# Kernel optimization log

Hardware: AMD Instinct MI355X
Metric: run time of the kernel (lower is better)

## Reference

```python
import jax, jax.numpy as jnp
import numpy as np

B, LT, D, H, DI = 8, 128, 512, 8, 2048
NMEM, LMEM = 1024, 64
DH = D // H
EPS = 1e-5
NEG = -1e9

def _ln(x, g, b):
    mu = x.mean(-1, keepdims=True)
    var = ((x - mu) ** 2).mean(-1, keepdims=True)
    return (x - mu) * jax.lax.rsqrt(var + EPS) * g + b

def _ffn(x, W1, b1, W2, b2):
    # PositionwiseFF with residual=True (dropout=0 / eval)
    return x + jax.nn.relu(x @ W1 + b1) @ W2 + b2

def setup_inputs():
    key = jax.random.key(0)
    ks = jax.random.split(key, 16)
    w = lambda i, shape: jax.random.normal(ks[i], shape, jnp.float32) * 0.02
    return {
        "dec_output": jax.random.normal(ks[0], (B, LT, D), jnp.float32),
        "mem_attn_out": jax.random.normal(ks[1], (B, LT, NMEM + 1), jnp.float32),
        "enc_out_mem": jax.random.normal(ks[2], (NMEM, LMEM, D), jnp.float32),
        "tgt_emb_mem": jax.random.normal(ks[3], (NMEM, LMEM, D), jnp.float32),
        "tgt_mask_mem": jax.random.randint(ks[4], (NMEM, LMEM), 0, 2, jnp.int32),
        "tgt_mask": jax.random.randint(ks[5], (B, LT), 0, 2, jnp.int32),
        "g0": jnp.ones((D,), jnp.float32), "be0": jnp.zeros((D,), jnp.float32),
        "g1": jnp.ones((D,), jnp.float32), "be1": jnp.zeros((D,), jnp.float32),
        "Wq": w(6, (D, D)), "bq": jnp.zeros((D,), jnp.float32),
        "Wk": w(7, (D, D)), "bk": jnp.zeros((D,), jnp.float32),
        "Wv": w(8, (D, D)), "bv": jnp.zeros((D,), jnp.float32),
        "Wo": w(9, (D, D)), "bo": jnp.zeros((D,), jnp.float32),
        "f1W1": w(10, (D, DI)), "f1b1": jnp.zeros((DI,), jnp.float32),
        "f1W2": w(11, (DI, D)), "f1b2": jnp.zeros((D,), jnp.float32),
        "f2W1": w(12, (D, DI)), "f2b1": jnp.zeros((DI,), jnp.float32),
        "f2W2": w(13, (DI, D)), "f2b2": jnp.zeros((D,), jnp.float32),
    }

def reference(dec_output, mem_attn_out, enc_out_mem, tgt_emb_mem, tgt_mask_mem, tgt_mask,
              g0, be0, g1, be1, Wq, bq, Wk, bk, Wv, bv, Wo, bo,
              f1W1, f1b1, f1W2, f1b2, f2W1, f2b1, f2W2, f2b2):
    x = _ln(dec_output, g0, be0)                       # [B,LT,D]
    N = B * LT
    samples = jnp.argmax(mem_attn_out, -1).reshape(N) - 1   # [-1, NMEM-1]
    valid = samples >= 0                               # [N]
    s = jnp.maximum(samples, 0)                        # clamp; masked later
    q = x.reshape(N, 1, D)
    # gather memory per selected query (torch compacts via unique; same math)
    k_in = enc_out_mem[s]                              # [N,LMEM,D]
    v_in = tgt_emb_mem[s]                              # [N,LMEM,D]
    kmask = tgt_mask_mem[s] != 0                       # True = valid key
    # multi-head attention, residual=True
    qh = (q @ Wq + bq).reshape(N, 1, H, DH).transpose(0, 2, 1, 3)     # [N,H,1,DH]
    kh = (k_in @ Wk + bk).reshape(N, LMEM, H, DH).transpose(0, 2, 1, 3)
    vh = (v_in @ Wv + bv).reshape(N, LMEM, H, DH).transpose(0, 2, 1, 3)
    scores = jnp.einsum('nhqd,nhkd->nhqk', qh, kh) / (DH ** 0.5)      # [N,H,1,LMEM]
    scores = jnp.where(kmask[:, None, None, :], scores, NEG)
    attn = jax.nn.softmax(scores, axis=-1)
    ctx = jnp.einsum('nhqk,nhkd->nhqd', attn, vh).transpose(0, 2, 1, 3).reshape(N, 1, D)
    st = q + ctx @ Wo + bo
    st = _ffn(st, f1W1, f1b1, f1W2, f1b2)
    st = _ln(st, g1, be1)
    # scatter back: positions with sample == -1 get zeros
    st = jnp.where(valid[:, None, None], st, 0.0)
    dec = x + st.reshape(B, LT, D)
    dec = _ffn(dec, f2W1, f2b1, f2W2, f2b2)
    return dec
```

## Files before the change

kernel.cpp:

```cpp
#include <hip/hip_runtime.h>
#include <math.h>

#define NQ   1024
#define DIM  512
#define NH   8
#define DHD  64
#define DFF  2048
#define LM   64

typedef __bf16 bf16x8 __attribute__((ext_vector_type(8)));
typedef float  f32x4  __attribute__((ext_vector_type(4)));

__device__ __forceinline__ unsigned short f2bf(float f) {
    unsigned u = __builtin_bit_cast(unsigned, f);
    return (unsigned short)((u + 0x7fffu + ((u >> 16) & 1u)) >> 16);
}
__device__ __forceinline__ float bflo(unsigned p) {
    return __builtin_bit_cast(float, p << 16);
}
__device__ __forceinline__ float bfhi(unsigned p) {
    return __builtin_bit_cast(float, p & 0xffff0000u);
}

__device__ __forceinline__ void gload16(const void* g, void* l) {
    __builtin_amdgcn_global_load_lds(
        (const __attribute__((address_space(1))) unsigned*)g,
        (__attribute__((address_space(3))) unsigned*)l, 16, 0, 0);
}

__device__ __forceinline__ float blk_sum(float v, volatile float* red) {
#pragma unroll
    for (int o = 32; o; o >>= 1) v += __shfl_down(v, o);
    __syncthreads();
    if ((threadIdx.x & 63) == 0) red[threadIdx.x >> 6] = v;
    __syncthreads();
    return red[0] + red[1] + red[2] + red[3];
}

__global__ __launch_bounds__(256) void ln0_argmax_k(
    const float* __restrict__ dec_out, const float* __restrict__ attn_out,
    const float* __restrict__ g, const float* __restrict__ be,
    float* __restrict__ x, unsigned* __restrict__ xb, int* __restrict__ samples)
{
    __shared__ float red[4];
    __shared__ float rv[4]; __shared__ int ri[4];
    const int n = blockIdx.x, t = threadIdx.x;

    float2 v = ((const float2*)(dec_out + (size_t)n * DIM))[t];
    float mu  = blk_sum(v.x + v.y, red) * (1.f / DIM);
    float dx = v.x - mu, dy = v.y - mu;
    float var = blk_sum(dx * dx + dy * dy, red) * (1.f / DIM);
    float rs = rsqrtf(var + 1e-5f);
    float2 gg = ((const float2*)g)[t], bb = ((const float2*)be)[t];
    float ox = dx * rs * gg.x + bb.x, oy = dy * rs * gg.y + bb.y;
    ((float2*)(x + (size_t)n * DIM))[t] = make_float2(ox, oy);
    xb[(size_t)n * 256 + t] = (unsigned)f2bf(ox) | ((unsigned)f2bf(oy) << 16);

    const float* ar = attn_out + (size_t)n * 1025;
    float bv = -INFINITY; int bi = 0x7fffffff;
    for (int i = t; i < 1025; i += 256) {
        float val = ar[i];
        if (val > bv || (val == bv && i < bi)) { bv = val; bi = i; }
    }
#pragma unroll
    for (int o = 32; o; o >>= 1) {
        float ov = __shfl_down(bv, o); int oi = __shfl_down(bi, o);
        if (ov > bv || (ov == bv && oi < bi)) { bv = ov; bi = oi; }
    }
    if ((t & 63) == 0) { rv[t >> 6] = bv; ri[t >> 6] = bi; }
    __syncthreads();
    if (t == 0) {
#pragma unroll
        for (int w = 1; w < 4; ++w)
            if (rv[w] > bv || (rv[w] == bv && ri[w] < bi)) { bv = rv[w]; bi = ri[w]; }
        samples[n] = bi - 1;
    }
}

struct PrepPtrs {
    const float* src[8];
    unsigned short* dst[8];
};
__global__ __launch_bounds__(256) void prep_weights_k(PrepPtrs p) {
    __shared__ float tile[32][33];
    const int bid = blockIdx.x;
    int m, lt;
    if (bid < 1024) { m = bid >> 8; lt = bid & 255; }
    else { m = 4 + ((bid - 1024) >> 10); lt = (bid - 1024) & 1023; }
    const int RS = (m < 4) ? 512 : ((m == 5 || m == 7) ? 2048 : 512);
    const int CS = (m < 4) ? 512 : ((m == 5 || m == 7) ? 512 : 2048);
    const int TC = CS >> 5;
    const int tr = lt / TC, tc = lt % TC;
    const float* s = p.src[m];
    unsigned short* d = p.dst[m];
    const int tx = threadIdx.x & 31, ty = threadIdx.x >> 5;
    if (m == 1) {
#pragma unroll
        for (int i = 0; i < 32; i += 8) {
            size_t idx = (size_t)(tr * 32 + ty + i) * CS + tc * 32 + tx;
            d[idx] = f2bf(s[idx]);
        }
    } else {
#pragma unroll
        for (int i = 0; i < 32; i += 8)
            tile[ty + i][tx] = s[(size_t)(tr * 32 + ty + i) * CS + tc * 32 + tx];
        __syncthreads();
#pragma unroll
        for (int i = 0; i < 32; i += 8)
            d[(size_t)(tc * 32 + ty + i) * RS + tr * 32 + tx] = f2bf(tile[tx][ty + i]);
    }
}

template<bool RELU, bool BIAS, bool RES, bool WF32, bool WBF>
__global__ __launch_bounds__(256) void mfma_gemm(
    const unsigned short* __restrict__ A, const unsigned short* __restrict__ Bt,
    float* __restrict__ Cf, unsigned short* __restrict__ Cb,
    const float* __restrict__ bias, const float* __restrict__ res,
    int K, int lda, int ldb, int ldc,
    int sA, int sB, int sC, int sBias)
{
    __shared__ unsigned short Ab[2][64 * 64];
    __shared__ unsigned short Bb[2][64 * 64];
    const int t = threadIdx.x, lane = t & 63, wid = t >> 6;
    const int bm = blockIdx.y * 64, bn = blockIdx.x * 64, bz = blockIdx.z;
    const unsigned short* Abase = A + (size_t)bz * sA + (size_t)bm * lda;
    const unsigned short* Bbase = Bt + (size_t)bz * sB + (size_t)bn * ldb;

    const int r0 = wid * 16 + (lane >> 3);
    const int cbs = lane & 7;

#define STAGE_T(buf, base, ld, kt)                                              \
    {                                                                           \
        int r_ = r0;                                                            \
        gload16(base + (size_t)r_ * ld + (kt) * 64 + ((cbs ^ (r_ & 7)) << 3),   \
                &buf[(wid * 2 + 0) * 512]);                                     \
        r_ = r0 + 8;                                                            \
        gload16(base + (size_t)r_ * ld + (kt) * 64 + ((cbs ^ (r_ & 7)) << 3),   \
                &buf[(wid * 2 + 1) * 512]);                                     \
    }

    const int lr = lane & 15, lg = lane >> 4;
    const int wr = (wid >> 1) * 32, wc = (wid & 1) * 32;
    const int mA0 = wr + lr, mA1 = wr + 16 + lr;
    const int nB0 = wc + lr, nB1 = wc + 16 + lr;
    f32x4 acc[2][2] = {};

#define COMPUTE(b)                                                              \
    _Pragma("unroll")                                                           \
    for (int kk = 0; kk < 2; ++kk) {                                            \
        const int kb = kk * 4 + lg;                                             \
        bf16x8 a0 = *(const bf16x8*)&Ab[b][mA0 * 64 + ((kb ^ (mA0 & 7)) << 3)]; \
        bf16x8 a1 = *(const bf16x8*)&Ab[b][mA1 * 64 + ((kb ^ (mA1 & 7)) << 3)]; \
        bf16x8 b0 = *(const bf16x8*)&Bb[b][nB0 * 64 + ((kb ^ (nB0 & 7)) << 3)]; \
        bf16x8 b1 = *(const bf16x8*)&Bb[b][nB1 * 64 + ((kb ^ (nB1 & 7)) << 3)]; \
        acc[0][0] = __builtin_amdgcn_mfma_f32_16x16x32_bf16(a0, b0, acc[0][0], 0, 0, 0); \
        acc[0][1] = __builtin_amdgcn_mfma_f32_16x16x32_bf16(a0, b1, acc[0][1], 0, 0, 0); \
        acc[1][0] = __builtin_amdgcn_mfma_f32_16x16x32_bf16(a1, b0, acc[1][0], 0, 0, 0); \
        acc[1][1] = __builtin_amdgcn_mfma_f32_16x16x32_bf16(a1, b1, acc[1][1], 0, 0, 0); \
    }

    STAGE_T(Ab[0], Abase, lda, 0);
    STAGE_T(Bb[0], Bbase, ldb, 0);
    __syncthreads();
    const int NT = K >> 6;
    int cur = 0;
    for (int kt = 0; kt < NT; ++kt) {
        if (kt + 1 < NT) {
            STAGE_T(Ab[cur ^ 1], Abase, lda, kt + 1);
            STAGE_T(Bb[cur ^ 1], Bbase, ldb, kt + 1);
        }
        if (cur == 0) { COMPUTE(0); } else { COMPUTE(1); }
        __syncthreads();
        cur ^= 1;
    }

#pragma unroll
    for (int fm = 0; fm < 2; ++fm)
#pragma unroll
    for (int fn = 0; fn < 2; ++fn) {
        const int col = bn + wc + fn * 16 + lr;
        float bia = BIAS ? bias[bz * sBias + col] : 0.f;
#pragma unroll
        for (int r = 0; r < 4; ++r) {
            const int row = bm + wr + fm * 16 + lg * 4 + r;
            const size_t ci = (size_t)bz * sC + (size_t)row * ldc + col;
            float v = acc[fm][fn][r] + bia;
            if (RES) v += res[(size_t)row * ldc + col];
            if (RELU) v = fmaxf(v, 0.f);
            if (WF32) Cf[ci] = v;
            if (WBF)  Cb[ci] = f2bf(v);
        }
    }
#undef STAGE_T
#undef COMPUTE
}

__global__ __launch_bounds__(256) void attn_mem_k(
    const float* __restrict__ qh, const unsigned short* __restrict__ u_bf,
    const float* __restrict__ enc, const float* __restrict__ vemb,
    const int* __restrict__ maskmem, const int* __restrict__ samples,
    const float* __restrict__ bk, unsigned* __restrict__ a_bf)
{
    __shared__ alignas(16) unsigned short U_lds[16 * 512];
    __shared__ float S_lds[8 * 68];
    __shared__ alignas(16) unsigned short P_lds[64 * 8];
    __shared__ float Cs_lds[8];
    __shared__ int Msk_lds[64];

    const int n = blockIdx.x, t = threadIdx.x;
    const int lane = t & 63, w = t >> 6;
    int s = samples[n]; if (s < 0) s = 0;

    {
        const uint4* ub = (const uint4*)(u_bf + (size_t)n * 4096);
#pragma unroll
        for (int i = 0; i < 4; ++i) {
            int chunk = t + i * 256;
            int h = chunk >> 6, c8 = chunk & 63;
            uint4 v = (h < 8) ? ub[chunk] : make_uint4(0, 0, 0, 0);
            *(uint4*)&U_lds[h * 512 + (c8 ^ (h & 7)) * 8] = v;
        }
        if (w == 0) Msk_lds[lane] = maskmem[(size_t)s * LM + lane];
        if (w == 1) {
            int h = lane >> 3, j = lane & 7;
            const float4* q4 = (const float4*)(qh + (size_t)n * DIM + h * 64 + j * 8);
            const float4* b4 = (const float4*)(bk + h * 64 + j * 8);
            float4 qa = q4[0], qb = q4[1], ba = b4[0], bb = b4[1];
            float c = qa.x * ba.x + qa.y * ba.y + qa.z * ba.z + qa.w * ba.w
                    + qb.x * bb.x + qb.y * bb.y + qb.z * bb.z + qb.w * bb.w;
            c += __shfl_xor(c, 1); c += __shfl_xor(c, 2); c += __shfl_xor(c, 4);
            if (j == 0) Cs_lds[h] = c;
        }
    }
    __syncthreads();

    {
        const float4* kb = (const float4*)(enc + (size_t)s * (LM * DIM));
        const int key = w * 16 + (lane & 15);
        const int lg = lane >> 4;
        const int h = lane & 15;
        const int base = key * 128 + lg * 2;
        f32x4 acc = {};
        float4 pf[4][2];
#pragma unroll
        for (int ss = 0; ss < 4; ++ss) {
            pf[ss][0] = kb[base + ss * 8];
            pf[ss][1] = kb[base + ss * 8 + 1];
        }
#pragma unroll
        for (int step = 0; step < 16; ++step) {
            float4 a0 = pf[step & 3][0], a1 = pf[step & 3][1];
            if (step + 4 < 16) {
                pf[step & 3][0] = kb[base + (step + 4) * 8];
                pf[step & 3][1] = kb[base + (step + 4) * 8 + 1];
            }
            bf16x8 af;
            af[0] = (__bf16)a0.x; af[1] = (__bf16)a0.y;
            af[2] = (__bf16)a0.z; af[3] = (__bf16)a0.w;
            af[4] = (__bf16)a1.x; af[5] = (__bf16)a1.y;
            af[6] = (__bf16)a1.z; af[7] = (__bf16)a1.w;
            const int c8 = step * 4 + lg;
            bf16x8 bfr = *(const bf16x8*)&U_lds[h * 512 + (c8 ^ (h & 7)) * 8];
            acc = __builtin_amdgcn_mfma_f32_16x16x32_bf16(af, bfr, acc, 0, 0, 0);
        }
        if (h < 8) {
#pragma unroll
            for (int r = 0; r < 4; ++r)
                S_lds[h * 68 + w * 16 + lg * 4 + r] = acc[r];
        }
    }
    __syncthreads();

#pragma unroll
    for (int hh = 0; hh < 2; ++hh) {
        const int h = w + hh * 4;
        float sc = (S_lds[h * 68 + lane] + Cs_lds[h]) * 0.125f;
        sc = (Msk_lds[lane] != 0) ? sc : -1e9f;
        float m = sc;
#pragma unroll
        for (int o = 32; o; o >>= 1) m = fmaxf(m, __shfl_xor(m, o));
        float e = __expf(sc - m);
        float su = e;
#pragma unroll
        for (int o = 32; o; o >>= 1) su += __shfl_xor(su, o);
        P_lds[lane * 8 + h] = f2bf(e / su);
    }
    __syncthreads();

    {
        float2 acc8[8];
#pragma unroll
        for (int h = 0; h < 8; ++h) acc8[h] = make_float2(0.f, 0.f);
        const float2* vb = (const float2*)(vemb + (size_t)s * (LM * DIM)) + t;
#pragma unroll 8
        for (int k = 0; k < 64; ++k) {
            float2 v = vb[k * 256];
            uint4 pr = *(const uint4*)&P_lds[k * 8];
            float p0 = bflo(pr.x), p1 = bfhi(pr.x);
            float p2 = bflo(pr.y), p3 = bfhi(pr.y);
            float p4 = bflo(pr.z), p5 = bfhi(pr.z);
            float p6 = bflo(pr.w), p7 = bfhi(pr.w);
            acc8[0].x = fmaf(p0, v.x, acc8[0].x); acc8[0].y = fmaf(p0, v.y, acc8[0].y);
            acc8[1].x = fmaf(p1, v.x, acc8[1].x); acc8[1].y = fmaf(p1, v.y, acc8[1].y);
            acc8[2].x = fmaf(p2, v.x, acc8[2].x); acc8[2].y = fmaf(p2, v.y, acc8[2].y);
            acc8[3].x = fmaf(p3, v.x, acc8[3].x); acc8[3].y = fmaf(p3, v.y, acc8[3].y);
            acc8[4].x = fmaf(p4, v.x, acc8[4].x); acc8[4].y = fmaf(p4, v.y, acc8[4].y);
            acc8[5].x = fmaf(p5, v.x, acc8[5].x); acc8[5].y = fmaf(p5, v.y, acc8[5].y);
            acc8[6].x = fmaf(p6, v.x, acc8[6].x); acc8[6].y = fmaf(p6, v.y, acc8[6].y);
            acc8[7].x = fmaf(p7, v.x, acc8[7].x); acc8[7].y = fmaf(p7, v.y, acc8[7].y);
        }
        unsigned* an = a_bf + (size_t)n * 2048;
#pragma unroll
        for (int h = 0; h < 8; ++h)
            an[h * 256 + t] = (unsigned)f2bf(acc8[h].x) | ((unsigned)f2bf(acc8[h].y) << 16);
    }
}

__global__ __launch_bounds__(256) void ln1_mask_add_k(
    const float* __restrict__ t1, const float* __restrict__ g,
    const float* __restrict__ be, const int* __restrict__ samples,
    const float* __restrict__ x, float* __restrict__ dec, unsigned* __restrict__ decb)
{
    __shared__ float red[4];
    const int n = blockIdx.x, t = threadIdx.x;
    float2 v = ((const float2*)(t1 + (size_t)n * DIM))[t];
    float mu  = blk_sum(v.x + v.y, red) * (1.f / DIM);
    float dx = v.x - mu, dy = v.y - mu;
    float var = blk_sum(dx * dx + dy * dy, red) * (1.f / DIM);
    float rs = rsqrtf(var + 1e-5f);
    float2 gg = ((const float2*)g)[t], bb = ((const float2*)be)[t];
    float sx = dx * rs * gg.x + bb.x, sy = dy * rs * gg.y + bb.y;
    if (samples[n] < 0) { sx = 0.f; sy = 0.f; }
    float2 xx = ((const float2*)(x + (size_t)n * DIM))[t];
    float ox = xx.x + sx, oy = xx.y + sy;
    ((float2*)(dec + (size_t)n * DIM))[t] = make_float2(ox, oy);
    decb[(size_t)n * 256 + t] = (unsigned)f2bf(ox) | ((unsigned)f2bf(oy) << 16);
}

extern "C" void kernel_launch(void* const* d_in, const int* in_sizes, int n_in,
                              void* d_out, int out_size, void* d_ws, size_t ws_size,
                              hipStream_t stream)
{
    const float* dec_output = (const float*)d_in[0];
    const float* mem_attn   = (const float*)d_in[1];
    const float* enc_mem    = (const float*)d_in[2];
    const float* temb_mem   = (const float*)d_in[3];
    const int*   mask_mem   = (const int*)d_in[4];
    const float* g0  = (const float*)d_in[6];
    const float* be0 = (const float*)d_in[7];
    const float* g1  = (const float*)d_in[8];
    const float* be1 = (const float*)d_in[9];
    const float* Wq  = (const float*)d_in[10];
    const float* bq  = (const float*)d_in[11];
    const float* Wk  = (const float*)d_in[12];
    const float* bk  = (const float*)d_in[13];
    const float* Wv  = (const float*)d_in[14];
    const float* bv  = (const float*)d_in[15];
    const float* Wo  = (const float*)d_in[16];
    const float* bo  = (const float*)d_in[17];
    const float* f1W1 = (const float*)d_in[18];
    const float* f1b1 = (const float*)d_in[19];
    const float* f1W2 = (const float*)d_in[20];
    const float* f1b2 = (const float*)d_in[21];
    const float* f2W1 = (const float*)d_in[22];
    const float* f2b1 = (const float*)d_in[23];
    const float* f2W2 = (const float*)d_in[24];
    const float* f2b2 = (const float*)d_in[25];
    float* out = (float*)d_out;

    float* ws = (float*)d_ws;
    float*          x_f   = ws + 0;
    unsigned*       x_b   = (unsigned*)(ws + 524288);
    float*          qh_f  = ws + 786432;
    unsigned short* qh_b  = (unsigned short*)(ws + 1310720);
    unsigned short* u_b   = (unsigned short*)(ws + 1572864);
    unsigned short* a_b   = (unsigned short*)(ws + 3670016);
    unsigned short* wqt   = (unsigned short*)(ws + 5767168);
    unsigned short* wkc   = (unsigned short*)(ws + 5898240);
    unsigned short* wvt   = (unsigned short*)(ws + 6029312);
    unsigned short* wot   = (unsigned short*)(ws + 6160384);
    unsigned short* f1w1t = (unsigned short*)(ws + 6291456);
    unsigned short* f1w2t = (unsigned short*)(ws + 6815744);
    unsigned short* f2w1t = (unsigned short*)(ws + 7340032);
    unsigned short* f2w2t = (unsigned short*)(ws + 7864320);
    int*            smp   = (int*)(ws + 8388608);
    float*          st0_f = (float*)u_b + 0;
    unsigned short* st0_b = (unsigned short*)((float*)u_b + 524288);
    float*          t1_f  = (float*)u_b + 786432;
    float*          dec_f = (float*)u_b + 1310720;
    unsigned*       dec_b = (unsigned*)((float*)u_b + 1835008);
    unsigned short* h1_b  = a_b;
    unsigned short* h2_b  = (unsigned short*)((float*)a_b + 1048576);

    PrepPtrs pp;
    pp.src[0] = Wq;   pp.dst[0] = wqt;
    pp.src[1] = Wk;   pp.dst[1] = wkc;
    pp.src[2] = Wv;   pp.dst[2] = wvt;
    pp.src[3] = Wo;   pp.dst[3] = wot;
    pp.src[4] = f1W1; pp.dst[4] = f1w1t;
    pp.src[5] = f1W2; pp.dst[5] = f1w2t;
    pp.src[6] = f2W1; pp.dst[6] = f2w1t;
    pp.src[7] = f2W2; pp.dst[7] = f2w2t;
    prep_weights_k<<<5120, 256, 0, stream>>>(pp);
    ln0_argmax_k<<<NQ, 256, 0, stream>>>(dec_output, mem_attn, g0, be0, x_f, x_b, smp);
    mfma_gemm<false, true, false, true, true><<<dim3(8, 16, 1), 256, 0, stream>>>(
        (const unsigned short*)x_b, wqt, qh_f, qh_b, bq, nullptr,
        DIM, DIM, DIM, DIM, 0, 0, 0, 0);
    mfma_gemm<false, false, false, false, true><<<dim3(8, 16, NH), 256, 0, stream>>>(
        qh_b, wkc, nullptr, u_b, nullptr, nullptr,
        DHD, DIM, DIM, NH * DIM, DHD, DHD, DIM, 0);
    attn_mem_k<<<NQ, 256, 0, stream>>>(qh_f, u_b, enc_mem, temb_mem, mask_mem, smp,
                                       bk, (unsigned*)a_b);
    mfma_gemm<false, true, false, false, true><<<dim3(1, 16, NH), 256, 0, stream>>>(
        a_b, wvt, nullptr, qh_b, bv, nullptr,
        DIM, NH * DIM, DIM, DIM, DIM, DHD * DIM, DHD, DHD);
    mfma_gemm<false, true, true, true, true><<<dim3(8, 16, 1), 256, 0, stream>>>(
        qh_b, wot, st0_f, st0_b, bo, x_f, DIM, DIM, DIM, DIM, 0, 0, 0, 0);
    mfma_gemm<true, true, false, false, true><<<dim3(32, 16, 1), 256, 0, stream>>>(
        st0_b, f1w1t, nullptr, h1_b, f1b1, nullptr, DIM, DIM, DIM, DFF, 0, 0, 0, 0);
    mfma_gemm<false, true, true, true, false><<<dim3(8, 16, 1), 256, 0, stream>>>(
        h1_b, f1w2t, t1_f, nullptr, f1b2, st0_f, DFF, DFF, DFF, DIM, 0, 0, 0, 0);
    ln1_mask_add_k<<<NQ, 256, 0, stream>>>(t1_f, g1, be1, smp, x_f, dec_f, dec_b);
    mfma_gemm<true, true, false, false, true><<<dim3(32, 16, 1), 256, 0, stream>>>(
        (const unsigned short*)dec_b, f2w1t, nullptr, h2_b, f2b1, nullptr,
        DIM, DIM, DIM, DFF, 0, 0, 0, 0);
    mfma_gemm<false, true, true, true, false><<<dim3(8, 16, 1), 256, 0, stream>>>(
        h2_b, f2w2t, out, nullptr, f2b2, dec_f, DFF, DFF, DFF, DIM, 0, 0, 0, 0);

    (void)in_sizes; (void)n_in; (void)out_size; (void)ws_size;
}
```

Baseline: 162.7 us.

## Split memory attention into parallel score and PV kernels, split-K FFN down-projection

Merges the weight-prep and LN0/argmax kernels into a single launch. Splits the per-query memory attention into a scores kernel and a softmax-plus-PV kernel, each with two blocks per query (halved head dims / output columns), so the grid has twice as many blocks. Splits the first FFN's K=2048 down-projection into two K halves writing partial sums, which the LN1 kernel adds together with the residual and bias. The intent is more parallelism on the many-CU GPU, paid for with extra global traffic for partial scores and partial outputs and one additional kernel launch.

```diff
diff --git a/kernel.cpp b/kernel.cpp
--- a/kernel.cpp
+++ b/kernel.cpp
@@ -37,15 +37,51 @@
     return red[0] + red[1] + red[2] + red[3];
 }
 
-__global__ __launch_bounds__(256) void ln0_argmax_k(
+struct PrepPtrs {
+    const float* src[8];
+    unsigned short* dst[8];
+};
+__global__ __launch_bounds__(256) void prep_ln0_k(
+    PrepPtrs p,
     const float* __restrict__ dec_out, const float* __restrict__ attn_out,
     const float* __restrict__ g, const float* __restrict__ be,
     float* __restrict__ x, unsigned* __restrict__ xb, int* __restrict__ samples)
 {
+    __shared__ float tile[32][33];
     __shared__ float red[4];
     __shared__ float rv[4]; __shared__ int ri[4];
-    const int n = blockIdx.x, t = threadIdx.x;
-
+    const int bid = blockIdx.x;
+
+    if (bid < 5120) {
+        int m, lt;
+        if (bid < 1024) { m = bid >> 8; lt = bid & 255; }
+        else { m = 4 + ((bid - 1024) >> 10); lt = (bid - 1024) & 1023; }
+        const int RS = (m < 4) ? 512 : ((m == 5 || m == 7) ? 2048 : 512);
+        const int CS = (m < 4) ? 512 : ((m == 5 || m == 7) ? 512 : 2048);
+        const int TC = CS >> 5;
+        const int tr = lt / TC, tc = lt % TC;
+        const float* s = p.src[m];
+        unsigned short* d = p.dst[m];
+        const int tx = threadIdx.x & 31, ty = threadIdx.x >> 5;
+        if (m == 1) {
+#pragma unroll
+            for (int i = 0; i < 32; i += 8) {
+                size_t idx = (size_t)(tr * 32 + ty + i) * CS + tc * 32 + tx;
+                d[idx] = f2bf(s[idx]);
+            }
+        } else {
+#pragma unroll
+            for (int i = 0; i < 32; i += 8)
+                tile[ty + i][tx] = s[(size_t)(tr * 32 + ty + i) * CS + tc * 32 + tx];
+            __syncthreads();
+#pragma unroll
+            for (int i = 0; i < 32; i += 8)
+                d[(size_t)(tc * 32 + ty + i) * RS + tr * 32 + tx] = f2bf(tile[tx][ty + i]);
+        }
+        return;
+    }
+
+    const int n = bid - 5120, t = threadIdx.x;
     float2 v = ((const float2*)(dec_out + (size_t)n * DIM))[t];
     float mu  = blk_sum(v.x + v.y, red) * (1.f / DIM);
     float dx = v.x - mu, dy = v.y - mu;
@@ -74,40 +110,6 @@
         for (int w = 1; w < 4; ++w)
             if (rv[w] > bv || (rv[w] == bv && ri[w] < bi)) { bv = rv[w]; bi = ri[w]; }
         samples[n] = bi - 1;
-    }
-}
-
-struct PrepPtrs {
-    const float* src[8];
-    unsigned short* dst[8];
-};
-__global__ __launch_bounds__(256) void prep_weights_k(PrepPtrs p) {
-    __shared__ float tile[32][33];
-    const int bid = blockIdx.x;
-    int m, lt;
-    if (bid < 1024) { m = bid >> 8; lt = bid & 255; }
-    else { m = 4 + ((bid - 1024) >> 10); lt = (bid - 1024) & 1023; }
-    const int RS = (m < 4) ? 512 : ((m == 5 || m == 7) ? 2048 : 512);
-    const int CS = (m < 4) ? 512 : ((m == 5 || m == 7) ? 512 : 2048);
-    const int TC = CS >> 5;
-    const int tr = lt / TC, tc = lt % TC;
-    const float* s = p.src[m];
-    unsigned short* d = p.dst[m];
-    const int tx = threadIdx.x & 31, ty = threadIdx.x >> 5;
-    if (m == 1) {
-#pragma unroll
-        for (int i = 0; i < 32; i += 8) {
-            size_t idx = (size_t)(tr * 32 + ty + i) * CS + tc * 32 + tx;
-            d[idx] = f2bf(s[idx]);
-        }
-    } else {
-#pragma unroll
-        for (int i = 0; i < 32; i += 8)
-            tile[ty + i][tx] = s[(size_t)(tr * 32 + ty + i) * CS + tc * 32 + tx];
-        __syncthreads();
-#pragma unroll
-        for (int i = 0; i < 32; i += 8)
-            d[(size_t)(tc * 32 + ty + i) * RS + tr * 32 + tx] = f2bf(tile[tx][ty + i]);
     }
 }
 
@@ -195,86 +197,85 @@
 #undef COMPUTE
 }
 
-__global__ __launch_bounds__(256) void attn_mem_k(
+__global__ __launch_bounds__(256) void attn_scores_k(
     const float* __restrict__ qh, const unsigned short* __restrict__ u_bf,
-    const float* __restrict__ enc, const float* __restrict__ vemb,
-    const int* __restrict__ maskmem, const int* __restrict__ samples,
-    const float* __restrict__ bk, unsigned* __restrict__ a_bf)
-{
-    __shared__ alignas(16) unsigned short U_lds[16 * 512];
-    __shared__ float S_lds[8 * 68];
-    __shared__ alignas(16) unsigned short P_lds[64 * 8];
+    const float* __restrict__ enc, const int* __restrict__ samples,
+    const float* __restrict__ bk, float* __restrict__ s_part)
+{
     __shared__ float Cs_lds[8];
-    __shared__ int Msk_lds[64];
-
-    const int n = blockIdx.x, t = threadIdx.x;
+    const int n = blockIdx.x, half = blockIdx.y, t = threadIdx.x;
     const int lane = t & 63, w = t >> 6;
     int s = samples[n]; if (s < 0) s = 0;
 
-    {
-        const uint4* ub = (const uint4*)(u_bf + (size_t)n * 4096);
-#pragma unroll
-        for (int i = 0; i < 4; ++i) {
-            int chunk = t + i * 256;
-            int h = chunk >> 6, c8 = chunk & 63;
-            uint4 v = (h < 8) ? ub[chunk] : make_uint4(0, 0, 0, 0);
-            *(uint4*)&U_lds[h * 512 + (c8 ^ (h & 7)) * 8] = v;
+    const float4* kb = (const float4*)(enc + (size_t)s * (LM * DIM));
+    const int key = w * 16 + (lane & 15);
+    const int lg = lane >> 4;
+    const int h = lane & 15;
+    const int base = key * 128 + half * 64 + lg * 2;
+    float4 pf[4][2];
+#pragma unroll
+    for (int ss = 0; ss < 4; ++ss) {
+        pf[ss][0] = kb[base + ss * 8];
+        pf[ss][1] = kb[base + ss * 8 + 1];
+    }
+
+    if (w == 1) {
+        int hq = lane >> 3, j = lane & 7;
+        const float4* q4 = (const float4*)(qh + (size_t)n * DIM + hq * 64 + j * 8);
+        const float4* b4 = (const float4*)(bk + hq * 64 + j * 8);
+        float4 qa = q4[0], qb = q4[1], ba = b4[0], bb = b4[1];
+        float c = qa.x * ba.x + qa.y * ba.y + qa.z * ba.z + qa.w * ba.w
+                + qb.x * bb.x + qb.y * bb.y + qb.z * bb.z + qb.w * bb.w;
+        c += __shfl_xor(c, 1); c += __shfl_xor(c, 2); c += __shfl_xor(c, 4);
+        if (j == 0) Cs_lds[hq] = c;
+    }
+
+    const unsigned short* ub = u_bf + (size_t)n * 4096 + (size_t)(h & 7) * 512 + half * 256;
+    f32x4 acc = {};
+#pragma unroll
+    for (int step = 0; step < 8; ++step) {
+        float4 a0 = pf[step & 3][0], a1 = pf[step & 3][1];
+        if (step + 4 < 8) {
+            pf[step & 3][0] = kb[base + (step + 4) * 8];
+            pf[step & 3][1] = kb[base + (step + 4) * 8 + 1];
         }
-        if (w == 0) Msk_lds[lane] = maskmem[(size_t)s * LM + lane];
-        if (w == 1) {
-            int h = lane >> 3, j = lane & 7;
-            const float4* q4 = (const float4*)(qh + (size_t)n * DIM + h * 64 + j * 8);
-            const float4* b4 = (const float4*)(bk + h * 64 + j * 8);
-            float4 qa = q4[0], qb = q4[1], ba = b4[0], bb = b4[1];
-            float c = qa.x * ba.x + qa.y * ba.y + qa.z * ba.z + qa.w * ba.w
-                    + qb.x * bb.x + qb.y * bb.y + qb.z * bb.z + qb.w * bb.w;
-            c += __shfl_xor(c, 1); c += __shfl_xor(c, 2); c += __shfl_xor(c, 4);
-            if (j == 0) Cs_lds[h] = c;
-        }
-    }
-    __syncthreads();
-
-    {
-        const float4* kb = (const float4*)(enc + (size_t)s * (LM * DIM));
-        const int key = w * 16 + (lane & 15);
-        const int lg = lane >> 4;
-        const int h = lane & 15;
-        const int base = key * 128 + lg * 2;
-        f32x4 acc = {};
-        float4 pf[4][2];
-#pragma unroll
-        for (int ss = 0; ss < 4; ++ss) {
-            pf[ss][0] = kb[base + ss * 8];
-            pf[ss][1] = kb[base + ss * 8 + 1];
-        }
-#pragma unroll
-        for (int step = 0; step < 16; ++step) {
-            float4 a0 = pf[step & 3][0], a1 = pf[step & 3][1];
-            if (step + 4 < 16) {
-                pf[step & 3][0] = kb[base + (step + 4) * 8];
-                pf[step & 3][1] = kb[base + (step + 4) * 8 + 1];
-            }
-            bf16x8 af;
-            af[0] = (__bf16)a0.x; af[1] = (__bf16)a0.y;
-            af[2] = (__bf16)a0.z; af[3] = (__bf16)a0.w;
-            af[4] = (__bf16)a1.x; af[5] = (__bf16)a1.y;
-            af[6] = (__bf16)a1.z; af[7] = (__bf16)a1.w;
-            const int c8 = step * 4 + lg;
-            bf16x8 bfr = *(const bf16x8*)&U_lds[h * 512 + (c8 ^ (h & 7)) * 8];
-            acc = __builtin_amdgcn_mfma_f32_16x16x32_bf16(af, bfr, acc, 0, 0, 0);
-        }
-        if (h < 8) {
-#pragma unroll
-            for (int r = 0; r < 4; ++r)
-                S_lds[h * 68 + w * 16 + lg * 4 + r] = acc[r];
-        }
-    }
+        bf16x8 af;
+        af[0] = (__bf16)a0.x; af[1] = (__bf16)a0.y;
+        af[2] = (__bf16)a0.z; af[3] = (__bf16)a0.w;
+        af[4] = (__bf16)a1.x; af[5] = (__bf16)a1.y;
+        af[6] = (__bf16)a1.z; af[7] = (__bf16)a1.w;
+        bf16x8 bfr = *(const bf16x8*)&ub[(step * 4 + lg) * 8];
+        acc = __builtin_amdgcn_mfma_f32_16x16x32_bf16(af, bfr, acc, 0, 0, 0);
+    }
+    __syncthreads();
+    if (h < 8) {
+        float cs = (half == 0) ? Cs_lds[h] : 0.f;
+        float* sp = s_part + (((size_t)n * 2 + half) * 8 + h) * 64 + w * 16 + lg * 4;
+        *(float4*)sp = make_float4(acc[0] + cs, acc[1] + cs, acc[2] + cs, acc[3] + cs);
+    }
+}
+
+__global__ __launch_bounds__(256) void attn_pv_k(
+    const float* __restrict__ s_part, const float* __restrict__ vemb,
+    const int* __restrict__ maskmem, const int* __restrict__ samples,
+    unsigned* __restrict__ a_bf)
+{
+    __shared__ float Sp_lds[1024];
+    __shared__ uint4 P_lds[64];
+    __shared__ float2 Red[8][128];
+    __shared__ int Msk_lds[64];
+    const int n = blockIdx.x, dh = blockIdx.y, t = threadIdx.x;
+    const int lane = t & 63, w = t >> 6;
+    int s = samples[n]; if (s < 0) s = 0;
+
+    ((float4*)Sp_lds)[t] = ((const float4*)(s_part + (size_t)n * 1024))[t];
+    if (t < 64) Msk_lds[t] = maskmem[(size_t)s * LM + t];
     __syncthreads();
 
 #pragma unroll
     for (int hh = 0; hh < 2; ++hh) {
         const int h = w + hh * 4;
-        float sc = (S_lds[h * 68 + lane] + Cs_lds[h]) * 0.125f;
+        float sc = (Sp_lds[h * 64 + lane] + Sp_lds[512 + h * 64 + lane]) * 0.125f;
         sc = (Msk_lds[lane] != 0) ? sc : -1e9f;
         float m = sc;
 #pragma unroll
@@ -283,47 +284,62 @@
         float su = e;
 #pragma unroll
         for (int o = 32; o; o >>= 1) su += __shfl_xor(su, o);
-        P_lds[lane * 8 + h] = f2bf(e / su);
-    }
-    __syncthreads();
-
-    {
-        float2 acc8[8];
-#pragma unroll
-        for (int h = 0; h < 8; ++h) acc8[h] = make_float2(0.f, 0.f);
-        const float2* vb = (const float2*)(vemb + (size_t)s * (LM * DIM)) + t;
+        ((unsigned short*)P_lds)[lane * 8 + h] = f2bf(e / su);
+    }
+    __syncthreads();
+
+    const int c = t & 127, kh = t >> 7;
+    const float2* vb = (const float2*)(vemb + (size_t)s * (LM * DIM)) + dh * 128 + c;
+    float2 acc8[8];
+#pragma unroll
+    for (int hh = 0; hh < 8; ++hh) acc8[hh] = make_float2(0.f, 0.f);
 #pragma unroll 8
-        for (int k = 0; k < 64; ++k) {
-            float2 v = vb[k * 256];
-            uint4 pr = *(const uint4*)&P_lds[k * 8];
-            float p0 = bflo(pr.x), p1 = bfhi(pr.x);
-            float p2 = bflo(pr.y), p3 = bfhi(pr.y);
-            float p4 = bflo(pr.z), p5 = bfhi(pr.z);
-            float p6 = bflo(pr.w), p7 = bfhi(pr.w);
-            acc8[0].x = fmaf(p0, v.x, acc8[0].x); acc8[0].y = fmaf(p0, v.y, acc8[0].y);
-            acc8[1].x = fmaf(p1, v.x, acc8[1].x); acc8[1].y = fmaf(p1, v.y, acc8[1].y);
-            acc8[2].x = fmaf(p2, v.x, acc8[2].x); acc8[2].y = fmaf(p2, v.y, acc8[2].y);
-            acc8[3].x = fmaf(p3, v.x, acc8[3].x); acc8[3].y = fmaf(p3, v.y, acc8[3].y);
-            acc8[4].x = fmaf(p4, v.x, acc8[4].x); acc8[4].y = fmaf(p4, v.y, acc8[4].y);
-            acc8[5].x = fmaf(p5, v.x, acc8[5].x); acc8[5].y = fmaf(p5, v.y, acc8[5].y);
-            acc8[6].x = fmaf(p6, v.x, acc8[6].x); acc8[6].y = fmaf(p6, v.y, acc8[6].y);
-            acc8[7].x = fmaf(p7, v.x, acc8[7].x); acc8[7].y = fmaf(p7, v.y, acc8[7].y);
+    for (int i = 0; i < 32; ++i) {
+        const int k = kh * 32 + i;
+        float2 v = vb[(size_t)k * 256];
+        uint4 pr = P_lds[k];
+        float p0 = bflo(pr.x), p1 = bfhi(pr.x);
+        float p2 = bflo(pr.y), p3 = bfhi(pr.y);
+        float p4 = bflo(pr.z), p5 = bfhi(pr.z);
+        float p6 = bflo(pr.w), p7 = bfhi(pr.w);
+        acc8[0].x = fmaf(p0, v.x, acc8[0].x); acc8[0].y = fmaf(p0, v.y, acc8[0].y);
+        acc8[1].x = fmaf(p1, v.x, acc8[1].x); acc8[1].y = fmaf(p1, v.y, acc8[1].y);
+        acc8[2].x = fmaf(p2, v.x, acc8[2].x); acc8[2].y = fmaf(p2, v.y, acc8[2].y);
+        acc8[3].x = fmaf(p3, v.x, acc8[3].x); acc8[3].y = fmaf(p3, v.y, acc8[3].y);
+        acc8[4].x = fmaf(p4, v.x, acc8[4].x); acc8[4].y = fmaf(p4, v.y, acc8[4].y);
+        acc8[5].x = fmaf(p5, v.x, acc8[5].x); acc8[5].y = fmaf(p5, v.y, acc8[5].y);
+        acc8[6].x = fmaf(p6, v.x, acc8[6].x); acc8[6].y = fmaf(p6, v.y, acc8[6].y);
+        acc8[7].x = fmaf(p7, v.x, acc8[7].x); acc8[7].y = fmaf(p7, v.y, acc8[7].y);
+    }
+    if (kh == 1) {
+#pragma unroll
+        for (int hh = 0; hh < 8; ++hh) Red[hh][c] = acc8[hh];
+    }
+    __syncthreads();
+    if (kh == 0) {
+        unsigned* an = a_bf + (size_t)n * 2048 + dh * 128;
+#pragma unroll
+        for (int hh = 0; hh < 8; ++hh) {
+            float2 r = Red[hh][c];
+            float ox = acc8[hh].x + r.x, oy = acc8[hh].y + r.y;
+            an[hh * 256 + c] = (unsigned)f2bf(ox) | ((unsigned)f2bf(oy) << 16);
         }
-        unsigned* an = a_bf + (size_t)n * 2048;
-#pragma unroll
-        for (int h = 0; h < 8; ++h)
-            an[h * 256 + t] = (unsigned)f2bf(acc8[h].x) | ((unsigned)f2bf(acc8[h].y) << 16);
     }
 }
 
 __global__ __launch_bounds__(256) void ln1_mask_add_k(
-    const float* __restrict__ t1, const float* __restrict__ g,
+    const float* __restrict__ t1p, const float* __restrict__ st0,
+    const float* __restrict__ b2, const float* __restrict__ g,
     const float* __restrict__ be, const int* __restrict__ samples,
     const float* __restrict__ x, float* __restrict__ dec, unsigned* __restrict__ decb)
 {
     __shared__ float red[4];
     const int n = blockIdx.x, t = threadIdx.x;
-    float2 v = ((const float2*)(t1 + (size_t)n * DIM))[t];
+    float2 p0 = ((const float2*)(t1p + (size_t)n * DIM))[t];
+    float2 p1 = ((const float2*)(t1p + (size_t)(NQ + n) * DIM))[t];
+    float2 s0 = ((const float2*)(st0 + (size_t)n * DIM))[t];
+    float2 b2v = ((const float2*)b2)[t];
+    float2 v = make_float2(p0.x + p1.x + s0.x + b2v.x, p0.y + p1.y + s0.y + b2v.y);
     float mu  = blk_sum(v.x + v.y, red) * (1.f / DIM);
     float dx = v.x - mu, dy = v.y - mu;
     float var = blk_sum(dx * dx + dy * dy, red) * (1.f / DIM);
@@ -384,9 +400,10 @@
     unsigned short* f2w1t = (unsigned short*)(ws + 7340032);
     unsigned short* f2w2t = (unsigned short*)(ws + 7864320);
     int*            smp   = (int*)(ws + 8388608);
+    float*          s_prt = ws + 8392704;
+    float*          t1p_f = ws + 9441280;
     float*          st0_f = (float*)u_b + 0;
     unsigned short* st0_b = (unsigned short*)((float*)u_b + 524288);
-    float*          t1_f  = (float*)u_b + 786432;
     float*          dec_f = (float*)u_b + 1310720;
     unsigned*       dec_b = (unsigned*)((float*)u_b + 1835008);
     unsigned short* h1_b  = a_b;
@@ -401,16 +418,17 @@
     pp.src[5] = f1W2; pp.dst[5] = f1w2t;
     pp.src[6] = f2W1; pp.dst[6] = f2w1t;
     pp.src[7] = f2W2; pp.dst[7] = f2w2t;
-    prep_weights_k<<<5120, 256, 0, stream>>>(pp);
-    ln0_argmax_k<<<NQ, 256, 0, stream>>>(dec_output, mem_attn, g0, be0, x_f, x_b, smp);
+    prep_ln0_k<<<5120 + NQ, 256, 0, stream>>>(pp, dec_output, mem_attn, g0, be0,
+                                              x_f, x_b, smp);
     mfma_gemm<false, true, false, true, true><<<dim3(8, 16, 1), 256, 0, stream>>>(
         (const unsigned short*)x_b, wqt, qh_f, qh_b, bq, nullptr,
         DIM, DIM, DIM, DIM, 0, 0, 0, 0);
     mfma_gemm<false, false, false, false, true><<<dim3(8, 16, NH), 256, 0, stream>>>(
         qh_b, wkc, nullptr, u_b, nullptr, nullptr,
         DHD, DIM, DIM, NH * DIM, DHD, DHD, DIM, 0);
-    attn_mem_k<<<NQ, 256, 0, stream>>>(qh_f, u_b, enc_mem, temb_mem, mask_mem, smp,
-                                       bk, (unsigned*)a_b);
+    attn_scores_k<<<dim3(NQ, 2), 256, 0, stream>>>(qh_f, u_b, enc_mem, smp, bk, s_prt);
+    attn_pv_k<<<dim3(NQ, 2), 256, 0, stream>>>(s_prt, temb_mem, mask_mem, smp,
+                                               (unsigned*)a_b);
     mfma_gemm<false, true, false, false, true><<<dim3(1, 16, NH), 256, 0, stream>>>(
         a_b, wvt, nullptr, qh_b, bv, nullptr,
         DIM, NH * DIM, DIM, DIM, DIM, DHD * DIM, DHD, DHD);
@@ -418,9 +436,11 @@
         qh_b, wot, st0_f, st0_b, bo, x_f, DIM, DIM, DIM, DIM, 0, 0, 0, 0);
     mfma_gemm<true, true, false, false, true><<<dim3(32, 16, 1), 256, 0, stream>>>(
         st0_b, f1w1t, nullptr, h1_b, f1b1, nullptr, DIM, DIM, DIM, DFF, 0, 0, 0, 0);
-    mfma_gemm<false, true, true, true, false><<<dim3(8, 16, 1), 256, 0, stream>>>(
-        h1_b, f1w2t, t1_f, nullptr, f1b2, st0_f, DFF, DFF, DFF, DIM, 0, 0, 0, 0);
-    ln1_mask_add_k<<<NQ, 256, 0, stream>>>(t1_f, g1, be1, smp, x_f, dec_f, dec_b);
+    mfma_gemm<false, false, false, true, false><<<dim3(8, 16, 2), 256, 0, stream>>>(
+        h1_b, f1w2t, t1p_f, nullptr, nullptr, nullptr,
+        1024, DFF, DFF, DIM, 1024, 1024, NQ * DIM, 0);
+    ln1_mask_add_k<<<NQ, 256, 0, stream>>>(t1p_f, st0_f, f1b2, g1, be1, smp,
+                                           x_f, dec_f, dec_b);
     mfma_gemm<true, true, false, false, true><<<dim3(32, 16, 1), 256, 0, stream>>>(
         (const unsigned short*)dec_b, f2w1t, nullptr, h2_b, f2b1, nullptr,
         DIM, DIM, DIM, DFF, 0, 0, 0, 0);
```

Result: faster. 157.2 us (-3.4%).
